# Kernel optimization log

Measured on AMD Instinct MI355X. Metric: run time of the kernel, lower is better.

## Reference

```python
import jax, jax.numpy as jnp
import numpy as np

B, S, D, H = 16, 784, 768, 12
DH = D // H  # 64


def rotate_half(x):
    # (x1, x2, x3, x4) -> (-x2, x1, -x4, x3), interleaved
    x_even = x[..., ::2]
    x_odd = x[..., 1::2]
    return jnp.stack((-x_odd, x_even), axis=-1).reshape(x.shape)


def setup_inputs() -> dict:
    key = jax.random.key(0)
    ks = jax.random.split(key, 12)
    s = 0.02
    return {
        "hidden_states": jax.random.normal(ks[0], (B, S, D), jnp.float32),
        "rotary_pos_emb": jax.random.uniform(ks[1], (B, S, DH), jnp.float32) * 6.28,
        "wq": jax.random.normal(ks[2], (D, D), jnp.float32) * s,
        "bq": jax.random.normal(ks[3], (D,), jnp.float32) * s,
        "wk": jax.random.normal(ks[4], (D, D), jnp.float32) * s,
        "bk": jax.random.normal(ks[5], (D,), jnp.float32) * s,
        "wv": jax.random.normal(ks[6], (D, D), jnp.float32) * s,
        "bv": jax.random.normal(ks[7], (D,), jnp.float32) * s,
        "wo": jax.random.normal(ks[8], (D, D), jnp.float32) * s,
        "bo": jax.random.normal(ks[9], (D,), jnp.float32) * s,
    }


def reference(hidden_states, rotary_pos_emb, wq, bq, wk, bk, wv, bv, wo, bo):
    scale = DH ** -0.5
    # Linear: x @ W^T + b; reshape to [B, H, S, DH]
    def proj(w, b):
        y = jnp.einsum("bsd,ed->bse", hidden_states, w) + b
        return y.reshape(B, S, H, DH).transpose(0, 2, 1, 3)

    q = proj(wq, bq)
    k = proj(wk, bk)
    v = proj(wv, bv)

    # RoPE: freqs [B, S, DH] -> [B, 1, S, DH] broadcast over heads
    cos = jnp.cos(rotary_pos_emb)[:, None, :, :]
    sin = jnp.sin(rotary_pos_emb)[:, None, :, :]
    q = q * cos + rotate_half(q) * sin
    k = k * cos + rotate_half(k) * sin

    attn = jnp.einsum("bhqd,bhkd->bhqk", q, k) * scale
    attn = jax.nn.softmax(attn, axis=-1)
    out = jnp.einsum("bhqk,bhkd->bhqd", attn, v)
    out = out.transpose(0, 2, 1, 3).reshape(B, S, D)
    out = jnp.einsum("bsd,ed->bse", out, wo) + bo
    return out
```

## Files before the change

### kernel.cpp

```cpp
#include <hip/hip_runtime.h>
#include <cstdint>
#include <cstddef>

constexpr int kB  = 16;
constexpr int kS  = 784;
constexpr int kD  = 768;
constexpr int kH  = 12;
constexpr int kM  = kB * kS;
constexpr int kSP = 832;

typedef __attribute__((ext_vector_type(8))) short bf16x8;
typedef __attribute__((ext_vector_type(4))) float floatx4;

__device__ __forceinline__ unsigned short f2bf(float x) {
    union { float f; unsigned int u; } v; v.f = x;
    unsigned int r = v.u + 0x7fffu + ((v.u >> 16) & 1u);
    return (unsigned short)(r >> 16);
}
__device__ __forceinline__ float bf2f(unsigned short h) {
    union { unsigned int u; float f; } v; v.u = ((unsigned int)h) << 16;
    return v.f;
}

__device__ __forceinline__ void gload_lds16(const void* g, void* l) {
    __builtin_amdgcn_global_load_lds(
        (const __attribute__((address_space(1))) void*)g,
        (__attribute__((address_space(3))) void*)l,
        16, 0, 0);
}

constexpr int kHsF4   = (kM * kD) / 4;
constexpr int kWF4    = (kD * kD) / 4;
constexpr int kPreTot = kHsF4 + 4 * kWF4 + (kM * 64) / 4;

__global__ __launch_bounds__(256)
void convert_pre(const float* __restrict__ hs, const float* __restrict__ rot,
                 const float* __restrict__ wq, const float* __restrict__ wk,
                 const float* __restrict__ wv, const float* __restrict__ wo,
                 const float* __restrict__ bq, const float* __restrict__ bk,
                 const float* __restrict__ bv,
                 unsigned short* __restrict__ hsB, unsigned short* __restrict__ wB,
                 unsigned int* __restrict__ csT, float* __restrict__ biasC)
{
    const int i = blockIdx.x * 256 + threadIdx.x;
    if (i < kHsF4) {
        float4 v = ((const float4*)hs)[i];
        ushort4 o = { f2bf(v.x), f2bf(v.y), f2bf(v.z), f2bf(v.w) };
        ((ushort4*)hsB)[i] = o;
    } else if (i < kHsF4 + 4 * kWF4) {
        const int j = i - kHsF4;
        const int w = j / kWF4, jj = j - w * kWF4;
        const float* src = (w == 0) ? wq : (w == 1) ? wk : (w == 2) ? wv : wo;
        float4 v = ((const float4*)src)[jj];
        ushort4 o = { f2bf(v.x), f2bf(v.y), f2bf(v.z), f2bf(v.w) };
        ((ushort4*)(wB + (size_t)w * (kD * kD)))[jj] = o;
    } else if (i < kPreTot) {
        const int j = i - kHsF4 - 4 * kWF4;
        float4 v = ((const float4*)rot)[j];
        float a[4] = { v.x, v.y, v.z, v.w };
        #pragma unroll
        for (int e = 0; e < 4; ++e) {
            float s, c;
            __sincosf(a[e], &s, &c);
            csT[j * 4 + e] = (unsigned)f2bf(c) | ((unsigned)f2bf(s) << 16);
        }
    } else {
        const int j = i - kPreTot;
        if (j < 3 * kD)
            biasC[j] = (j < kD) ? bq[j] : (j < 2 * kD) ? bk[j - kD] : bv[j - 2 * kD];
    }
}

enum { MODE_QKV = 0, MODE_OUT = 1 };

#define BARR  __builtin_amdgcn_s_barrier()
#define LGK0  asm volatile("s_waitcnt lgkmcnt(0)" ::: "memory")
#define VM4   asm volatile("s_waitcnt vmcnt(4)" ::: "memory")
#define VM0   asm volatile("s_waitcnt vmcnt(0)" ::: "memory")
#define PRIO1 __builtin_amdgcn_s_setprio(1)
#define PRIO0 __builtin_amdgcn_s_setprio(0)

#define LDA4(KS, RB, MQ) do{ \
  afr[0]=*(const bf16x8*)(rdA##KS+(RB)+((MQ)+0)*4096); \
  afr[1]=*(const bf16x8*)(rdA##KS+(RB)+((MQ)+1)*4096); \
  afr[2]=*(const bf16x8*)(rdA##KS+(RB)+((MQ)+2)*4096); \
  afr[3]=*(const bf16x8*)(rdA##KS+(RB)+((MQ)+3)*4096); }while(0)

#define LDB4(KS, RB) do{ \
  bfr[0]=*(const bf16x8*)(rdB##KS+(RB)); \
  bfr[1]=*(const bf16x8*)(rdB##KS+(RB)+8192); \
  bfr[2]=*(const bf16x8*)(rdB##KS+(RB)+16384); \
  bfr[3]=*(const bf16x8*)(rdB##KS+(RB)+24576); }while(0)

#define MFMA16(MQ) do{ _Pragma("unroll") for(int nt=0;nt<4;++nt){ \
  acc[(MQ)  ][nt]=__builtin_amdgcn_mfma_f32_16x16x32_bf16(afr[0],bfr[nt],acc[(MQ)  ][nt],0,0,0); \
  acc[(MQ)+1][nt]=__builtin_amdgcn_mfma_f32_16x16x32_bf16(afr[1],bfr[nt],acc[(MQ)+1][nt],0,0,0); \
  acc[(MQ)+2][nt]=__builtin_amdgcn_mfma_f32_16x16x32_bf16(afr[2],bfr[nt],acc[(MQ)+2][nt],0,0,0); \
  acc[(MQ)+3][nt]=__builtin_amdgcn_mfma_f32_16x16x32_bf16(afr[3],bfr[nt],acc[(MQ)+3][nt],0,0,0); \
}}while(0)

#define KTILE(RB, SB, KT) do{ \
   LDA4(0, RB, 0); LDB4(0, RB); \
    if ((KT) <= 10) { stA(1, (KT)+1, SB); stB(1, (KT)+1, SB); } \
    BARR; LGK0; PRIO1; MFMA16(0); PRIO0; BARR; \
   LDA4(0, RB, 4); \
    BARR; LGK0; PRIO1; MFMA16(4); PRIO0; BARR; \
   LDA4(1, RB, 0); LDB4(1, RB); \
    BARR; LGK0; PRIO1; MFMA16(0); PRIO0; BARR; \
   LDA4(1, RB, 4); \
    if ((KT) <= 9) { stA(0, (KT)+2, RB); stB(0, (KT)+2, RB); VM4; } \
    else if ((KT) == 10) { VM0; } \
    BARR; LGK0; PRIO1; MFMA16(4); PRIO0; BARR; \
}while(0)

template<int MODE>
__global__ __launch_bounds__(512, 2)
void gemm8(const unsigned short* __restrict__ A, const unsigned short* __restrict__ W,
           const float* __restrict__ bias, const unsigned int* __restrict__ csT,
           unsigned short* __restrict__ Qp, unsigned short* __restrict__ Kp,
           unsigned short* __restrict__ Vtp, float* __restrict__ Op)
{
    constexpr int NTL = (MODE == MODE_QKV) ? 9 : 3;

    __shared__ unsigned short SM[65536];

    const int lin   = blockIdx.x;
    const int group = lin / (8 * NTL);
    const int rem   = lin - group * (8 * NTL);
    int m_tile, n_tile;
    if (group < 6) { m_tile = group * 8 + (rem & 7); n_tile = rem >> 3; }
    else           { m_tile = 48; n_tile = rem; }
    const int m0 = m_tile * 256;
    const int n0 = n_tile * 256;

    const int tid  = threadIdx.x;
    const int wave = tid >> 6;
    const int lane = tid & 63;
    const int quad = lane >> 4, l16 = lane & 15;
    const int wm = wave & 1;
    const int wn = wave >> 1;

    const int l8  = lane >> 3;
    const int sc  = (lane & 7) ^ l8;
    const unsigned short* gA0 = A + (size_t)(m0 + wave * 16 + l8) * kD + sc * 8;
    const unsigned short* gA1 = gA0 + (size_t)8 * kD;
    const unsigned short* gB0 = W + (size_t)(n0 + wave * 16 + l8) * kD + sc * 8;
    const unsigned short* gB1 = gB0 + (size_t)8 * kD;
    char* smc = (char*)SM;

    auto stA = [&](int h, int kt, int bufoff) {
        const int off = h * 98304 + kt * 64;
        gload_lds16(gA0 + off, smc + bufoff + h * 16384 + wave * 2048);
        gload_lds16(gA1 + off, smc + bufoff + h * 16384 + wave * 2048 + 1024);
    };
    auto stB = [&](int h, int kt, int bufoff) {
        const int off = h * 98304 + kt * 64;
        gload_lds16(gB0 + off, smc + 65536 + bufoff + h * 16384 + wave * 2048);
        gload_lds16(gB1 + off, smc + 65536 + bufoff + h * 16384 + wave * 2048 + 1024);
    };

    const int swz0 = ((quad    ) ^ (l16 & 7)) * 16;
    const int swz1 = ((quad + 4) ^ (l16 & 7)) * 16;
    const char* rdA0 = (const char*)SM + (wm * 16 + l16) * 128 + swz0;
    const char* rdA1 = (const char*)SM + (wm * 16 + l16) * 128 + swz1;
    const char* rdB0 = (const char*)SM + 65536 + (wn * 16 + l16) * 128 + swz0;
    const char* rdB1 = (const char*)SM + 65536 + (wn * 16 + l16) * 128 + swz1;

    floatx4 acc[8][4];
    #pragma unroll
    for (int m = 0; m < 8; ++m)
        #pragma unroll
        for (int nt = 0; nt < 4; ++nt)
            acc[m][nt] = {0.f, 0.f, 0.f, 0.f};
    bf16x8 afr[4], bfr[4];

    stA(0, 0, 0);      stB(0, 0, 0);
    stA(1, 0, 0);      stB(1, 0, 0);
    stA(0, 1, 32768);  stB(0, 1, 32768);
    VM4;
    BARR;

    #pragma unroll
    for (int ktp = 0; ktp < 6; ++ktp) {
        KTILE(0,     32768, ktp * 2);
        KTILE(32768, 0,     ktp * 2 + 1);
    }

    if constexpr (MODE == MODE_OUT) {
        #pragma unroll
        for (int nt = 0; nt < 4; ++nt) {
            const int n = n0 + nt * 64 + wn * 16 + l16;
            const float bv = bias[n];
            #pragma unroll
            for (int m = 0; m < 8; ++m)
                #pragma unroll
                for (int r = 0; r < 4; ++r) {
                    const int mm = m0 + m * 32 + wm * 16 + quad * 4 + r;
                    Op[(size_t)mm * kD + n] = acc[m][nt][r] + bv;
                }
        }
    } else {
        const int proj = n_tile / 3;
        if (proj < 2) {
            unsigned short* dst = proj ? Kp : Qp;
            const float scale = proj ? 1.0f : 0.125f * 1.44269504088896341f;
            #pragma unroll
            for (int nt = 0; nt < 4; ++nt) {
                const int n = n0 + nt * 64 + wn * 16 + l16;
                const float bv = bias[n];
                const int col = n - proj * kD;
                const int dh = col & 63;
                const int odd = l16 & 1;
                #pragma unroll
                for (int m = 0; m < 8; ++m)
                    #pragma unroll
                    for (int r = 0; r < 4; ++r) {
                        const int mm = m0 + m * 32 + wm * 16 + quad * 4 + r;
                        const float val = acc[m][nt][r] + bv;
                        const float px = __shfl_xor(val, 1);
                        const unsigned u = csT[(size_t)mm * 64 + dh];
                        const float c = bf2f((unsigned short)(u & 0xffffu));
                        const float s = bf2f((unsigned short)(u >> 16));
                        const float out = odd ? (val * c + px * s) : (val * c - px * s);
                        dst[(size_t)mm * kD + col] = f2bf(out * scale);
                    }
            }
        } else {
            #pragma unroll
            for (int nt = 0; nt < 4; ++nt) {
                const int n = n0 + nt * 64 + wn * 16 + l16;
                const float bv = bias[n];
                const int col = n - 2 * kD;
                const int h = col >> 6, dh = col & 63;
                #pragma unroll
                for (int m = 0; m < 8; ++m) {
                    const int m_r0 = m0 + m * 32 + wm * 16 + quad * 4;
                    const int b = m_r0 / kS;
                    const int s = m_r0 - b * kS;
                    ushort4 pk;
                    pk.x = f2bf(acc[m][nt][0] + bv);
                    pk.y = f2bf(acc[m][nt][1] + bv);
                    pk.z = f2bf(acc[m][nt][2] + bv);
                    pk.w = f2bf(acc[m][nt][3] + bv);
                    *(ushort4*)(Vtp + (size_t)((b * kH + h) * 64 + dh) * kSP + s) = pk;
                }
            }
        }
    }
}

__global__ __launch_bounds__(256)
void flash_attn(const unsigned short* __restrict__ Qg,
                const unsigned short* __restrict__ Kg,
                const unsigned short* __restrict__ Vtg,
                unsigned short* __restrict__ Og)
{
    __shared__ unsigned short KV[2][8192];
    __shared__ unsigned short Ps[4][32 * 68];

    const int lin   = blockIdx.x;
    const int group = lin / 56;
    const int rem   = lin - group * 56;
    const int bh = group * 8 + (rem & 7);
    const int qt = rem >> 3;
    const int b = bh / kH, h = bh - b * kH;
    const int tid = threadIdx.x, wave = tid >> 6, lane = tid & 63;
    const int quad = lane >> 4, l16 = lane & 15;
    const int q0 = qt * 128;
    const size_t rowBase = (size_t)(b * kS) * kD + h * 64;

    #pragma unroll
    for (int j = 0; j < 4; ++j) {
        const int idx = (wave * 4 + j) * 64 + lane;
        const int row = idx >> 3, slot = idx & 7, seg = slot ^ (row & 7);
        gload_lds16(Qg + rowBase + (size_t)(q0 + row) * kD + seg * 8,
                    &KV[0][(wave * 4 + j) * 512]);
    }
    __syncthreads();
    bf16x8 aq[2][2];
    #pragma unroll
    for (int mt = 0; mt < 2; ++mt)
        #pragma unroll
        for (int ch = 0; ch < 2; ++ch) {
            const int row = wave * 32 + mt * 16 + l16;
            const int slot = (ch * 4 + quad) ^ (row & 7);
            aq[mt][ch] = *(const bf16x8*)&KV[0][row * 64 + slot * 8];
        }
    __syncthreads();

    const int cidx0 = wave * 128 + lane;
    const int crow0 = cidx0 >> 3, cseg0 = (cidx0 & 7) ^ (crow0 & 7);
    const int cidx1 = cidx0 + 64;
    const int crow1 = cidx1 >> 3, cseg1 = (cidx1 & 7) ^ (crow1 & 7);

    {
        gload_lds16(Kg + rowBase + (size_t)(crow0)*kD + cseg0 * 8, &KV[0][wave * 1024]);
        gload_lds16(Vtg + (size_t)(bh * 64 + crow0) * kSP + cseg0 * 8, &KV[0][4096 + wave * 1024]);
        gload_lds16(Kg + rowBase + (size_t)(crow1)*kD + cseg1 * 8, &KV[0][wave * 1024 + 512]);
        gload_lds16(Vtg + (size_t)(bh * 64 + crow1) * kSP + cseg1 * 8, &KV[0][4096 + wave * 1024 + 512]);
    }

    floatx4 oacc[2][4];
    #pragma unroll
    for (int mt = 0; mt < 2; ++mt)
        #pragma unroll
        for (int nt = 0; nt < 4; ++nt)
            oacc[mt][nt] = {0.f, 0.f, 0.f, 0.f};
    floatx4 lsum[2];
    lsum[0] = {0.f, 0.f, 0.f, 0.f};
    lsum[1] = {0.f, 0.f, 0.f, 0.f};
    const bf16x8 onesb = { 16256, 16256, 16256, 16256,
                           16256, 16256, 16256, 16256 };

    for (int kt = 0; kt < 13; ++kt) {
        __syncthreads();
        if (kt < 12) {
            const int nb = (kt + 1) & 1;
            const int kr = (kt + 1) * 64;
            gload_lds16(Kg + rowBase + (size_t)(kr + crow0) * kD + cseg0 * 8,
                        &KV[nb][wave * 1024]);
            gload_lds16(Vtg + (size_t)(bh * 64 + crow0) * kSP + kr + cseg0 * 8,
                        &KV[nb][4096 + wave * 1024]);
            gload_lds16(Kg + rowBase + (size_t)(kr + crow1) * kD + cseg1 * 8,
                        &KV[nb][wave * 1024 + 512]);
            gload_lds16(Vtg + (size_t)(bh * 64 + crow1) * kSP + kr + cseg1 * 8,
                        &KV[nb][4096 + wave * 1024 + 512]);
        }
        const unsigned short* Ks = &KV[kt & 1][0];
        const unsigned short* Vs = &KV[kt & 1][4096];

        bf16x8 bk[4][2];
        #pragma unroll
        for (int nt = 0; nt < 4; ++nt)
            #pragma unroll
            for (int ch = 0; ch < 2; ++ch) {
                const int row = nt * 16 + l16;
                const int slot = (ch * 4 + quad) ^ (row & 7);
                bk[nt][ch] = *(const bf16x8*)&Ks[row * 64 + slot * 8];
            }

        floatx4 sc[2][4];
        __builtin_amdgcn_s_setprio(1);
        #pragma unroll
        for (int mt = 0; mt < 2; ++mt)
            #pragma unroll
            for (int nt = 0; nt < 4; ++nt) {
                sc[mt][nt] = {0.f, 0.f, 0.f, 0.f};
                sc[mt][nt] = __builtin_amdgcn_mfma_f32_16x16x32_bf16(
                    aq[mt][0], bk[nt][0], sc[mt][nt], 0, 0, 0);
                sc[mt][nt] = __builtin_amdgcn_mfma_f32_16x16x32_bf16(
                    aq[mt][1], bk[nt][1], sc[mt][nt], 0, 0, 0);
            }
        __builtin_amdgcn_s_setprio(0);

        if (kt == 12) {
            #pragma unroll
            for (int mt = 0; mt < 2; ++mt)
                #pragma unroll
                for (int nt = 1; nt < 4; ++nt)
                    #pragma unroll
                    for (int r = 0; r < 4; ++r) sc[mt][nt][r] = -1e30f;
        }

        #pragma unroll
        for (int mt = 0; mt < 2; ++mt)
            #pragma unroll
            for (int nt = 0; nt < 4; ++nt)
                #pragma unroll
                for (int r = 0; r < 4; ++r) {
                    union { float f; unsigned u; } pu;
                    pu.f = exp2f(sc[mt][nt][r]);
                    Ps[wave][(mt * 16 + quad * 4 + r) * 68 + nt * 16 + l16] =
                        (unsigned short)(pu.u >> 16);
                }

        bf16x8 ap[2][2];
        #pragma unroll
        for (int mt = 0; mt < 2; ++mt)
            #pragma unroll
            for (int ks = 0; ks < 2; ++ks)
                ap[mt][ks] = *(const bf16x8*)&Ps[wave][(mt * 16 + l16) * 68 + ks * 32 + quad * 8];

        __builtin_amdgcn_s_setprio(1);
        #pragma unroll
        for (int ks = 0; ks < 2; ++ks) {
            #pragma unroll
            for (int nt = 0; nt < 4; ++nt) {
                const int row = nt * 16 + l16;
                const int slot = (ks * 4 + quad) ^ (row & 7);
                const bf16x8 bv = *(const bf16x8*)&Vs[row * 64 + slot * 8];
                #pragma unroll
                for (int mt = 0; mt < 2; ++mt)
                    oacc[mt][nt] = __builtin_amdgcn_mfma_f32_16x16x32_bf16(
                        ap[mt][ks], bv, oacc[mt][nt], 0, 0, 0);
            }
            #pragma unroll
            for (int mt = 0; mt < 2; ++mt)
                lsum[mt] = __builtin_amdgcn_mfma_f32_16x16x32_bf16(
                    ap[mt][ks], onesb, lsum[mt], 0, 0, 0);
        }
        __builtin_amdgcn_s_setprio(0);
    }

    #pragma unroll
    for (int mt = 0; mt < 2; ++mt)
        #pragma unroll
        for (int r = 0; r < 4; ++r) {
            const int srow = q0 + wave * 32 + mt * 16 + quad * 4 + r;
            if (srow < kS) {
                const float inv = 1.0f / lsum[mt][r];
                #pragma unroll
                for (int nt = 0; nt < 4; ++nt)
                    Og[rowBase + (size_t)srow * kD + nt * 16 + l16] =
                        f2bf(oacc[mt][nt][r] * inv);
            }
        }
}

extern "C" void kernel_launch(void* const* d_in, const int* in_sizes, int n_in,
                              void* d_out, int out_size, void* d_ws, size_t ws_size,
                              hipStream_t stream)
{
    (void)in_sizes; (void)n_in; (void)out_size; (void)ws_size;
    const float* hs  = (const float*)d_in[0];
    const float* rot = (const float*)d_in[1];
    const float* wq  = (const float*)d_in[2];
    const float* bq  = (const float*)d_in[3];
    const float* wk  = (const float*)d_in[4];
    const float* bk  = (const float*)d_in[5];
    const float* wv  = (const float*)d_in[6];
    const float* bv  = (const float*)d_in[7];
    const float* wo  = (const float*)d_in[8];
    const float* bo  = (const float*)d_in[9];

    char* ws = (char*)d_ws;
    unsigned short* hsB  = (unsigned short*)ws;
    unsigned short* wB   = (unsigned short*)(ws + 19267584);
    unsigned int*   csT  = (unsigned int*)(ws + 23986176);
    float*          biasC= (float*)(ws + 27197440);
    unsigned short* Q    = (unsigned short*)(ws + 27206656);
    unsigned short* K    = (unsigned short*)(ws + 46474240);
    unsigned short* Vt   = (unsigned short*)(ws + 65741824);
    unsigned short* O    = hsB;

    convert_pre<<<dim3(12505), dim3(256), 0, stream>>>(hs, rot, wq, wk, wv, wo, bq, bk, bv,
                                                       hsB, wB, csT, biasC);
    gemm8<MODE_QKV><<<dim3(441), dim3(512), 0, stream>>>(
        hsB, wB, biasC, csT, Q, K, Vt, nullptr);
    flash_attn<<<dim3(7 * 192), dim3(256), 0, stream>>>(Q, K, Vt, O);
    gemm8<MODE_OUT><<<dim3(147), dim3(512), 0, stream>>>(
        O, wB + 3 * kD * kD, bo, nullptr, nullptr, nullptr, nullptr, (float*)d_out);
}
```

Measured before the change: 259.9 us.

## Triple-buffer K/V tiles in flash attention with explicit vmcnt waits

```diff
diff --git a/kernel.cpp b/kernel.cpp
--- a/kernel.cpp
+++ b/kernel.cpp
@@ -20,6 +20,14 @@
 __device__ __forceinline__ float bf2f(unsigned short h) {
     union { unsigned int u; float f; } v; v.u = ((unsigned int)h) << 16;
     return v.f;
+}
+
+__device__ __forceinline__ float fast_exp2(float x) {
+#if __has_builtin(__builtin_amdgcn_exp2f)
+    return __builtin_amdgcn_exp2f(x);
+#else
+    return __expf(x * 0.69314718055994531f);
+#endif
 }
 
 __device__ __forceinline__ void gload_lds16(const void* g, void* l) {
@@ -255,7 +263,7 @@
                 const unsigned short* __restrict__ Vtg,
                 unsigned short* __restrict__ Og)
 {
-    __shared__ unsigned short KV[2][8192];
+    __shared__ unsigned short KV[3][8192];
     __shared__ unsigned short Ps[4][32 * 68];
 
     const int lin   = blockIdx.x;
@@ -293,12 +301,20 @@
     const int cidx1 = cidx0 + 64;
     const int crow1 = cidx1 >> 3, cseg1 = (cidx1 & 7) ^ (crow1 & 7);
 
-    {
-        gload_lds16(Kg + rowBase + (size_t)(crow0)*kD + cseg0 * 8, &KV[0][wave * 1024]);
-        gload_lds16(Vtg + (size_t)(bh * 64 + crow0) * kSP + cseg0 * 8, &KV[0][4096 + wave * 1024]);
-        gload_lds16(Kg + rowBase + (size_t)(crow1)*kD + cseg1 * 8, &KV[0][wave * 1024 + 512]);
-        gload_lds16(Vtg + (size_t)(bh * 64 + crow1) * kSP + cseg1 * 8, &KV[0][4096 + wave * 1024 + 512]);
-    }
+    auto stage = [&](int kt, int buf) {
+        const int kr = kt * 64;
+        gload_lds16(Kg + rowBase + (size_t)(kr + crow0) * kD + cseg0 * 8,
+                    &KV[buf][wave * 1024]);
+        gload_lds16(Vtg + (size_t)(bh * 64 + crow0) * kSP + kr + cseg0 * 8,
+                    &KV[buf][4096 + wave * 1024]);
+        gload_lds16(Kg + rowBase + (size_t)(kr + crow1) * kD + cseg1 * 8,
+                    &KV[buf][wave * 1024 + 512]);
+        gload_lds16(Vtg + (size_t)(bh * 64 + crow1) * kSP + kr + cseg1 * 8,
+                    &KV[buf][4096 + wave * 1024 + 512]);
+    };
+
+    stage(0, 0);
+    stage(1, 1);
 
     floatx4 oacc[2][4];
     #pragma unroll
@@ -312,22 +328,18 @@
     const bf16x8 onesb = { 16256, 16256, 16256, 16256,
                            16256, 16256, 16256, 16256 };
 
+    int cur = 0;
+    int pre = 2;
     for (int kt = 0; kt < 13; ++kt) {
-        __syncthreads();
-        if (kt < 12) {
-            const int nb = (kt + 1) & 1;
-            const int kr = (kt + 1) * 64;
-            gload_lds16(Kg + rowBase + (size_t)(kr + crow0) * kD + cseg0 * 8,
-                        &KV[nb][wave * 1024]);
-            gload_lds16(Vtg + (size_t)(bh * 64 + crow0) * kSP + kr + cseg0 * 8,
-                        &KV[nb][4096 + wave * 1024]);
-            gload_lds16(Kg + rowBase + (size_t)(kr + crow1) * kD + cseg1 * 8,
-                        &KV[nb][wave * 1024 + 512]);
-            gload_lds16(Vtg + (size_t)(bh * 64 + crow1) * kSP + kr + cseg1 * 8,
-                        &KV[nb][4096 + wave * 1024 + 512]);
-        }
-        const unsigned short* Ks = &KV[kt & 1][0];
-        const unsigned short* Vs = &KV[kt & 1][4096];
+        asm volatile("s_barrier" ::: "memory");
+        if (kt < 11) stage(kt + 2, pre);
+        if (kt < 11)       asm volatile("s_waitcnt vmcnt(8)" ::: "memory");
+        else if (kt == 11) asm volatile("s_waitcnt vmcnt(4)" ::: "memory");
+        else               asm volatile("s_waitcnt vmcnt(0)" ::: "memory");
+        asm volatile("s_barrier" ::: "memory");
+
+        const unsigned short* Ks = &KV[cur][0];
+        const unsigned short* Vs = &KV[cur][4096];
 
         bf16x8 bk[4][2];
         #pragma unroll
@@ -369,7 +381,7 @@
                 #pragma unroll
                 for (int r = 0; r < 4; ++r) {
                     union { float f; unsigned u; } pu;
-                    pu.f = exp2f(sc[mt][nt][r]);
+                    pu.f = fast_exp2(sc[mt][nt][r]);
                     Ps[wave][(mt * 16 + quad * 4 + r) * 68 + nt * 16 + l16] =
                         (unsigned short)(pu.u >> 16);
                 }
@@ -400,6 +412,9 @@
                     ap[mt][ks], onesb, lsum[mt], 0, 0, 0);
         }
         __builtin_amdgcn_s_setprio(0);
+
+        cur = (cur == 2) ? 0 : cur + 1;
+        pre = (pre == 2) ? 0 : pre + 1;
     }
 
     #pragma unroll
```

Result: faster. 252.9 us (-2.7%).
